# Performance work log

Measured on AMD Instinct MI355X. Metric: run time of the kernel, lower is better.

The kernel has to match this reference:

```python
import jax, jax.numpy as jnp
import numpy as np

OUTH = 7
OUTW = 7


def setup_inputs() -> dict:
    key = jax.random.key(0)
    k1, k2 = jax.random.split(key)
    H, W, C, N = 512, 512, 256, 2000
    x = jax.random.normal(k1, (H, W, C), dtype=jnp.float32)
    # normalized roi corners in [0,1]; sort so that y0<=y1, x0<=x1
    p = jax.random.uniform(k2, (N, 2, 2), dtype=jnp.float32)
    lo = jnp.min(p, axis=1)   # [N,2] -> (y0, x0)
    hi = jnp.max(p, axis=1)   # [N,2] -> (y1, x1)
    rois = jnp.concatenate([lo, hi], axis=1)  # [N,4] = [y0,x0,y1,x1]
    return {"x": x, "rois": rois, "spatial_scale": 1}


def reference(x, rois, spatial_scale):
    # x: [H, W, C] feature map; rois: [N,4] normalized [y0,x0,y1,x1].
    # Per-ROI crop + adaptive average pool to (OUTH, OUTW), vectorized over
    # all ROIs via a 2D integral image (summed-area table).
    H, W, C = x.shape
    hs = jnp.floor(H * rois[:, 0]).astype(jnp.int32)  # [N]
    ws = jnp.floor(W * rois[:, 1]).astype(jnp.int32)
    he = jnp.floor(H * rois[:, 2]).astype(jnp.int32)
    we = jnp.floor(W * rois[:, 3]).astype(jnp.int32)
    # guarantee at least 1 pixel per ROI (original code would crash on empty)
    he = jnp.maximum(he, hs + 1)
    we = jnp.maximum(we, ws + 1)
    rh = he - hs  # [N] region heights
    rw = we - ws  # [N] region widths

    # AdaptiveAvgPool2d bin edges: start=floor(i*r/out), end=ceil((i+1)*r/out)
    i = jnp.arange(OUTH, dtype=jnp.int32)
    j = jnp.arange(OUTW, dtype=jnp.int32)
    hb0 = hs[:, None] + (i[None, :] * rh[:, None]) // OUTH            # [N,OUTH]
    hb1 = hs[:, None] + -((-(i[None, :] + 1) * rh[:, None]) // OUTH)  # ceil div
    wb0 = ws[:, None] + (j[None, :] * rw[:, None]) // OUTW            # [N,OUTW]
    wb1 = ws[:, None] + -((-(j[None, :] + 1) * rw[:, None]) // OUTW)

    # integral image S[a,b,:] = sum(x[:a,:b,:]); shape [H+1, W+1, C]
    S = jnp.cumsum(jnp.cumsum(x, axis=0), axis=1)
    S = jnp.pad(S, ((1, 0), (1, 0), (0, 0)))

    def gather(hi_, wi_):  # [N,OUTH],[N,OUTW] -> [N,OUTH,OUTW,C]
        return S[hi_[:, :, None], wi_[:, None, :], :]

    bin_sum = gather(hb1, wb1) - gather(hb0, wb1) - gather(hb1, wb0) + gather(hb0, wb0)
    area = ((hb1 - hb0)[:, :, None] * (wb1 - wb0)[:, None, :]).astype(x.dtype)
    return bin_sum / area[..., None]  # [N, OUTH, OUTW, C]
```

## Files before the change

kernel.cpp:

```cpp
#include <hip/hip_runtime.h>

#define Hdim 512
#define Wdim 512
#define Cdim 256
#define CQ 64
#define OUTH 7
#define OUTW 7
#define TS 16
#define NT 32
#define NROI_BINS (OUTH * OUTW)
#define QSCALE 8.0f

typedef short s16x4 __attribute__((ext_vector_type(4)));
typedef int   i32x4 __attribute__((ext_vector_type(4)));
typedef float f32x4 __attribute__((ext_vector_type(4)));

static constexpr size_t SLOC_ELEMS = (size_t)Hdim * Wdim * Cdim;
static constexpr size_t EL_ELEMS   = (size_t)Hdim * NT * Cdim;
static constexpr size_t F_ELEMS    = (size_t)NT * Wdim * Cdim;
static constexpr size_t WS_NEED    = (SLOC_ELEMS + EL_ELEMS + F_ELEMS) * sizeof(short);

__device__ __forceinline__ size_t spix(int h, int w) {
    return (size_t)(((h >> 4) * NT + (w >> 4)) * (TS * TS)
                    + ((h & 15) << 4) + (w & 15));
}

__global__ void local_sat(const float* __restrict__ x, short* __restrict__ S) {
    const int tJ = blockIdx.x & (NT - 1);
    const int tI = blockIdx.x >> 5;
    const int c  = threadIdx.x;

    const float* xp = x + ((size_t)(tI * TS) * Wdim + (size_t)(tJ * TS)) * Cdim + c;
    short* sp = S + (size_t)blockIdx.x * (TS * TS) * Cdim + c;

    int P[TS];
    #pragma unroll
    for (int w = 0; w < TS; ++w) P[w] = 0;

    #pragma unroll
    for (int h = 0; h < TS; ++h) {
        float v[TS];
        #pragma unroll
        for (int w = 0; w < TS; ++w)
            v[w] = __builtin_nontemporal_load(&xp[((size_t)h * Wdim + w) * Cdim]);
        int rowAcc = 0;
        #pragma unroll
        for (int w = 0; w < TS; ++w) {
            rowAcc += (int)rintf(v[w] * QSCALE);
            P[w] += rowAcc;
            sp[(size_t)(h * TS + w) * Cdim] = (short)P[w];
        }
    }
}

__global__ void make_eleft(const short* __restrict__ S, short* __restrict__ EL) {
    const int h = blockIdx.x;
    const int c = threadIdx.x;
    short* ep = EL + (size_t)h * NT * Cdim + c;

    int acc = 0;
    #pragma unroll
    for (int J = 0; J < NT; ++J) {
        const int t = S[spix(h, J * TS + TS - 1) * Cdim + c];
        ep[(size_t)J * Cdim] = (short)acc;
        acc += t;
    }
}

__global__ void make_f(const short* __restrict__ S, const short* __restrict__ EL,
                       short* __restrict__ F) {
    const int w = blockIdx.x;
    const int c = threadIdx.x;
    const int J = w >> 4;
    const short* ep = EL + (size_t)J * Cdim + c;
    short* fp = F + (size_t)w * Cdim + c;

    int acc = 0;
    #pragma unroll
    for (int I = 0; I < NT; ++I) {
        const int hb = I * TS + TS - 1;
        fp[(size_t)I * Wdim * Cdim] = (short)acc;
        acc += (int)S[spix(hb, w) * Cdim + c] + (int)ep[(size_t)hb * NT * Cdim];
    }
}

__device__ __forceinline__ void roi_bounds(const float4 r, int& hs, int& ws,
                                           int& rh, int& rw) {
    hs = (int)floorf((float)Hdim * r.x);
    ws = (int)floorf((float)Wdim * r.y);
    int he = (int)floorf((float)Hdim * r.z);
    int we = (int)floorf((float)Wdim * r.w);
    he = max(he, hs + 1);
    we = max(we, ws + 1);
    rh = he - hs;
    rw = we - ws;
}

__global__ __launch_bounds__(256) void gather_kernel(
        const s16x4* __restrict__ S, const s16x4* __restrict__ EL,
        const s16x4* __restrict__ F, const float4* __restrict__ rois,
        f32x4* __restrict__ out, int NB) {
    const int b = blockIdx.x * 4 + (threadIdx.x >> 6);
    const int q = threadIdx.x & 63;
    if (b >= NB) return;
    const int n = b / OUTH;
    const int i = b % OUTH;

    const float4 r = rois[n];
    int hs, ws, rh, rw;
    roi_bounds(r, hs, ws, rh, rw);

    const int hb0 = hs + (i * rh) / OUTH;
    const int hb1 = hs + ((i + 1) * rh + OUTH - 1) / OUTH;
    const float dh = (float)(hb1 - hb0);

    const int  h1 = hb1 - 1;
    const int  h0 = max(hb0 - 1, 0);
    const bool mh = (hb0 > 0);
    const int  I1 = h1 >> 4, I0 = h0 >> 4;

    const i32x4 z = {0, 0, 0, 0};
    f32x4* op = out + ((size_t)(n * OUTH + i) * OUTW) * CQ + q;

    #pragma unroll
    for (int j = 0; j < OUTW; ++j) {
        const int wb0 = ws + (j * rw) / OUTW;
        const int wb1 = ws + ((j + 1) * rw + OUTW - 1) / OUTW;
        const int w1 = wb1 - 1;
        const int w0 = max(wb0 - 1, 0);
        const bool mw = (wb0 > 0);
        const int J1 = w1 >> 4, J0 = w0 >> 4;

        const s16x4 a11 = S[spix(h1, w1) * CQ + q];
        const s16x4 a01 = S[spix(h0, w1) * CQ + q];
        const s16x4 a10 = S[spix(h1, w0) * CQ + q];
        const s16x4 a00 = S[spix(h0, w0) * CQ + q];
        const s16x4 g11 = F[((size_t)I1 * Wdim + w1) * CQ + q];
        const s16x4 g01 = F[((size_t)I0 * Wdim + w1) * CQ + q];
        const s16x4 g10 = F[((size_t)I1 * Wdim + w0) * CQ + q];
        const s16x4 g00 = F[((size_t)I0 * Wdim + w0) * CQ + q];
        const s16x4 e11 = EL[((size_t)h1 * NT + J1) * CQ + q];
        const s16x4 e01 = EL[((size_t)h0 * NT + J1) * CQ + q];
        const s16x4 e10 = EL[((size_t)h1 * NT + J0) * CQ + q];
        const s16x4 e00 = EL[((size_t)h0 * NT + J0) * CQ + q];

        const i32x4 s11 = __builtin_convertvector(a11, i32x4)
                        + __builtin_convertvector(g11, i32x4)
                        + __builtin_convertvector(e11, i32x4);
        const i32x4 s01 = mh ? (__builtin_convertvector(a01, i32x4)
                        + __builtin_convertvector(g01, i32x4)
                        + __builtin_convertvector(e01, i32x4)) : z;
        const i32x4 s10 = mw ? (__builtin_convertvector(a10, i32x4)
                        + __builtin_convertvector(g10, i32x4)
                        + __builtin_convertvector(e10, i32x4)) : z;
        const i32x4 s00 = (mh && mw) ? (__builtin_convertvector(a00, i32x4)
                        + __builtin_convertvector(g00, i32x4)
                        + __builtin_convertvector(e00, i32x4)) : z;

        const i32x4 d = ((s11 - s01) - s10) + s00;
        const float inv = 1.0f / (dh * (float)(wb1 - wb0) * QSCALE);
        const f32x4 o = __builtin_convertvector(d, f32x4) * inv;
        __builtin_nontemporal_store(o, &op[(size_t)j * CQ]);
    }
}

__global__ void direct_kernel(const float* __restrict__ x,
                              const float* __restrict__ rois,
                              float* __restrict__ out, int N) {
    const int bid = blockIdx.x;
    const int n = bid / NROI_BINS;
    const int rem = bid % NROI_BINS;
    const int i = rem / OUTW;
    const int j = rem % OUTW;
    const int c = threadIdx.x;
    if (n >= N) return;

    const float4 r = reinterpret_cast<const float4*>(rois)[n];
    int hs, ws, rh, rw;
    roi_bounds(r, hs, ws, rh, rw);

    const int hb0 = hs + (i * rh) / OUTH;
    const int hb1 = hs + ((i + 1) * rh + OUTH - 1) / OUTH;
    const int wb0 = ws + (j * rw) / OUTW;
    const int wb1 = ws + ((j + 1) * rw + OUTW - 1) / OUTW;

    double acc = 0.0;
    for (int h = hb0; h < hb1; ++h) {
        const float* xp = x + ((size_t)h * Wdim) * Cdim + c;
        for (int w = wb0; w < wb1; ++w)
            acc += (double)xp[(size_t)w * Cdim];
    }
    const float area = (float)((hb1 - hb0) * (wb1 - wb0));
    out[((size_t)bid) * Cdim + c] = (float)(acc / (double)area);
}

extern "C" void kernel_launch(void* const* d_in, const int* in_sizes, int n_in,
                              void* d_out, int out_size, void* d_ws, size_t ws_size,
                              hipStream_t stream) {
    const float* x    = (const float*)d_in[0];
    const float* rois = (const float*)d_in[1];
    float* out        = (float*)d_out;
    const int N       = in_sizes[1] / 4;

    if (ws_size >= WS_NEED) {
        short* Sloc = (short*)d_ws;
        short* EL   = Sloc + SLOC_ELEMS;
        short* F    = EL + EL_ELEMS;
        local_sat<<<NT * NT, Cdim, 0, stream>>>(x, Sloc);
        make_eleft<<<Hdim, Cdim, 0, stream>>>(Sloc, EL);
        make_f<<<Wdim, Cdim, 0, stream>>>(Sloc, EL, F);
        const int NB = N * OUTH;
        gather_kernel<<<(NB + 3) / 4, 256, 0, stream>>>(
            (const s16x4*)Sloc, (const s16x4*)EL, (const s16x4*)F,
            (const float4*)rois, (f32x4*)out, NB);
    } else {
        direct_kernel<<<N * NROI_BINS, Cdim, 0, stream>>>(x, rois, out, N);
    }
}
```

Measured before the change: 148.7 us.

## Split gather corner rows across half-waves with 16-byte loads and lane shuffle

In the gather kernel each wave is now split in two: lanes 0-31 read the bottom row corners (h1) and lanes 32-63 read the top row corners (h0). Each lane loads 8 channels at once (16-byte loads) instead of 4. The partial differences are combined with a cross-half __shfl_xor, and only the low half stores 8 floats. This halves the per-lane load count and widens memory transactions, at the cost of 8 shuffles per bin and idle store lanes.

```diff
diff --git a/kernel.cpp b/kernel.cpp
--- a/kernel.cpp
+++ b/kernel.cpp
@@ -3,7 +3,6 @@
 #define Hdim 512
 #define Wdim 512
 #define Cdim 256
-#define CQ 64
 #define OUTH 7
 #define OUTW 7
 #define TS 16
@@ -11,9 +10,9 @@
 #define NROI_BINS (OUTH * OUTW)
 #define QSCALE 8.0f
 
-typedef short s16x4 __attribute__((ext_vector_type(4)));
-typedef int   i32x4 __attribute__((ext_vector_type(4)));
-typedef float f32x4 __attribute__((ext_vector_type(4)));
+typedef short s16x8 __attribute__((ext_vector_type(8)));
+typedef int   i32x8 __attribute__((ext_vector_type(8)));
+typedef float f32x8 __attribute__((ext_vector_type(8)));
 
 static constexpr size_t SLOC_ELEMS = (size_t)Hdim * Wdim * Cdim;
 static constexpr size_t EL_ELEMS   = (size_t)Hdim * NT * Cdim;
@@ -96,13 +95,19 @@
     rw = we - ws;
 }
 
+__device__ __forceinline__ i32x8 ldw(const short* p) {
+    return __builtin_convertvector(*reinterpret_cast<const s16x8*>(p), i32x8);
+}
+
 __global__ __launch_bounds__(256) void gather_kernel(
-        const s16x4* __restrict__ S, const s16x4* __restrict__ EL,
-        const s16x4* __restrict__ F, const float4* __restrict__ rois,
-        f32x4* __restrict__ out, int NB) {
+        const short* __restrict__ S, const short* __restrict__ EL,
+        const short* __restrict__ F, const float4* __restrict__ rois,
+        float* __restrict__ out, int NB) {
     const int b = blockIdx.x * 4 + (threadIdx.x >> 6);
-    const int q = threadIdx.x & 63;
     if (b >= NB) return;
+    const int lane = threadIdx.x & 63;
+    const int cb   = (lane & 31) * 8;
+    const bool hiL = lane >= 32;
     const int n = b / OUTH;
     const int i = b % OUTH;
 
@@ -114,13 +119,15 @@
     const int hb1 = hs + ((i + 1) * rh + OUTH - 1) / OUTH;
     const float dh = (float)(hb1 - hb0);
 
-    const int  h1 = hb1 - 1;
-    const int  h0 = max(hb0 - 1, 0);
+    const int h1 = hb1 - 1;
+    const int h0 = max(hb0 - 1, 0);
     const bool mh = (hb0 > 0);
-    const int  I1 = h1 >> 4, I0 = h0 >> 4;
-
-    const i32x4 z = {0, 0, 0, 0};
-    f32x4* op = out + ((size_t)(n * OUTH + i) * OUTW) * CQ + q;
+
+    const int hh = hiL ? h0 : h1;
+    const int Ih = hh >> 4;
+    const i32x8 z = {0, 0, 0, 0, 0, 0, 0, 0};
+
+    float* op = out + ((size_t)(n * OUTH + i) * OUTW) * Cdim + cb;
 
     #pragma unroll
     for (int j = 0; j < OUTW; ++j) {
@@ -131,36 +138,28 @@
         const bool mw = (wb0 > 0);
         const int J1 = w1 >> 4, J0 = w0 >> 4;
 
-        const s16x4 a11 = S[spix(h1, w1) * CQ + q];
-        const s16x4 a01 = S[spix(h0, w1) * CQ + q];
-        const s16x4 a10 = S[spix(h1, w0) * CQ + q];
-        const s16x4 a00 = S[spix(h0, w0) * CQ + q];
-        const s16x4 g11 = F[((size_t)I1 * Wdim + w1) * CQ + q];
-        const s16x4 g01 = F[((size_t)I0 * Wdim + w1) * CQ + q];
-        const s16x4 g10 = F[((size_t)I1 * Wdim + w0) * CQ + q];
-        const s16x4 g00 = F[((size_t)I0 * Wdim + w0) * CQ + q];
-        const s16x4 e11 = EL[((size_t)h1 * NT + J1) * CQ + q];
-        const s16x4 e01 = EL[((size_t)h0 * NT + J1) * CQ + q];
-        const s16x4 e10 = EL[((size_t)h1 * NT + J0) * CQ + q];
-        const s16x4 e00 = EL[((size_t)h0 * NT + J0) * CQ + q];
-
-        const i32x4 s11 = __builtin_convertvector(a11, i32x4)
-                        + __builtin_convertvector(g11, i32x4)
-                        + __builtin_convertvector(e11, i32x4);
-        const i32x4 s01 = mh ? (__builtin_convertvector(a01, i32x4)
-                        + __builtin_convertvector(g01, i32x4)
-                        + __builtin_convertvector(e01, i32x4)) : z;
-        const i32x4 s10 = mw ? (__builtin_convertvector(a10, i32x4)
-                        + __builtin_convertvector(g10, i32x4)
-                        + __builtin_convertvector(e10, i32x4)) : z;
-        const i32x4 s00 = (mh && mw) ? (__builtin_convertvector(a00, i32x4)
-                        + __builtin_convertvector(g00, i32x4)
-                        + __builtin_convertvector(e00, i32x4)) : z;
-
-        const i32x4 d = ((s11 - s01) - s10) + s00;
-        const float inv = 1.0f / (dh * (float)(wb1 - wb0) * QSCALE);
-        const f32x4 o = __builtin_convertvector(d, f32x4) * inv;
-        __builtin_nontemporal_store(o, &op[(size_t)j * CQ]);
+        const i32x8 right = ldw(&S[spix(hh, w1) * Cdim + cb])
+                          + ldw(&F[((size_t)Ih * Wdim + w1) * Cdim + cb])
+                          + ldw(&EL[((size_t)hh * NT + J1) * Cdim + cb]);
+        const i32x8 left  = ldw(&S[spix(hh, w0) * Cdim + cb])
+                          + ldw(&F[((size_t)Ih * Wdim + w0) * Cdim + cb])
+                          + ldw(&EL[((size_t)hh * NT + J0) * Cdim + cb]);
+
+        const i32x8 t   = mw ? left : z;
+        const i32x8 val = hiL ? (mh ? (t - right) : z) : (right - t);
+
+        i32x8 other;
+        #pragma unroll
+        for (int k = 0; k < 8; ++k)
+            other[k] = __shfl_xor(val[k], 32, 64);
+        const i32x8 d = val + other;
+
+        if (!hiL) {
+            const float inv = 1.0f / (dh * (float)(wb1 - wb0) * QSCALE);
+            const f32x8 o = __builtin_convertvector(d, f32x8) * inv;
+            __builtin_nontemporal_store(o,
+                reinterpret_cast<f32x8*>(&op[(size_t)j * Cdim]));
+        }
     }
 }
 
@@ -211,8 +210,7 @@
         make_f<<<Wdim, Cdim, 0, stream>>>(Sloc, EL, F);
         const int NB = N * OUTH;
         gather_kernel<<<(NB + 3) / 4, 256, 0, stream>>>(
-            (const s16x4*)Sloc, (const s16x4*)EL, (const s16x4*)F,
-            (const float4*)rois, (f32x4*)out, NB);
+            Sloc, EL, F, (const float4*)rois, out, NB);
     } else {
         direct_kernel<<<N * NROI_BINS, Cdim, 0, stream>>>(x, rois, out, N);
     }
```

Result: slower. 155.5 us (+4.6%).
